# Performance work log

Hardware: AMD Instinct MI355X
Metric: run time of the kernel (lower is better)

Reference implementation:

```python
import jax, jax.numpy as jnp
from jax import lax
import numpy as np

H = 20  # hidden_size


def _lstm_layer(x, Wih, Whh, bih, bhh):
    # x: [B, T, D_in]; Wih: [4H, D_in]; Whh: [4H, H]
    B = x.shape[0]
    b = bih + bhh  # [4H]

    def step(carry, xt):
        h, c = carry
        gates = xt @ Wih.T + h @ Whh.T + b  # [B, 4H]
        i, f, g, o = jnp.split(gates, 4, axis=-1)  # torch gate order: i,f,g,o
        i = jax.nn.sigmoid(i)
        f = jax.nn.sigmoid(f)
        g = jnp.tanh(g)
        o = jax.nn.sigmoid(o)
        c = f * c + i * g
        h = o * jnp.tanh(c)
        return (h, c), h

    h0 = jnp.zeros((B, H), x.dtype)
    c0 = jnp.zeros((B, H), x.dtype)
    (_, _), hs = lax.scan(step, (h0, c0), jnp.swapaxes(x, 0, 1))  # hs: [T, B, H]
    return jnp.swapaxes(hs, 0, 1)  # [B, T, H]


def setup_inputs() -> dict:
    key = jax.random.key(0)
    ks = jax.random.split(key, 11)
    B, T, D = 4096, 512, 1
    s = 1.0 / np.sqrt(H)  # torch LSTM init scale
    u = lambda k, shp: jax.random.uniform(k, shp, jnp.float32, -s, s)
    return {
        "x": jax.random.normal(ks[0], (B, T, D), jnp.float32),
        "Wih0": u(ks[1], (4 * H, D)),
        "Whh0": u(ks[2], (4 * H, H)),
        "bih0": u(ks[3], (4 * H,)),
        "bhh0": u(ks[4], (4 * H,)),
        "Wih1": u(ks[5], (4 * H, H)),
        "Whh1": u(ks[6], (4 * H, H)),
        "bih1": u(ks[7], (4 * H,)),
        "bhh1": u(ks[8], (4 * H,)),
        "fcW": u(ks[9], (1, H)),
        "fcb": u(ks[10], (1,)),
    }


def reference(x, Wih0, Whh0, bih0, bhh0, Wih1, Whh1, bih1, bhh1, fcW, fcb):
    h1 = _lstm_layer(x, Wih0, Whh0, bih0, bhh0)   # [B, T, H]
    h2 = _lstm_layer(h1, Wih1, Whh1, bih1, bhh1)  # [B, T, H]
    # self.drop is defined but never applied in the original forward
    return h2[:, -1, :] @ fcW.T + fcb  # [B, 1]
```

## Files before the change

kernel.cpp:

```cpp
#include <hip/hip_runtime.h>
#include <hip/hip_bf16.h>


namespace {
constexpr int H_  = 20;
constexpr int T_  = 512;
constexpr int B_  = 4096;
constexpr int GPB = 3;

__device__ __forceinline__ float sigm(float v) {
    return 1.0f / (1.0f + __expf(-v));
}
__device__ __forceinline__ float tanh_fast(float v) {
    return 1.0f - 2.0f / (1.0f + __expf(2.0f * v));
}
}

__global__ __launch_bounds__(256, 3) void lstm2_fc_kernel(
    const float* __restrict__ x,
    const float* __restrict__ Wih0, const float* __restrict__ Whh0,
    const float* __restrict__ bih0, const float* __restrict__ bhh0,
    const float* __restrict__ Wih1, const float* __restrict__ Whh1,
    const float* __restrict__ bih1, const float* __restrict__ bhh1,
    const float* __restrict__ fcW,  const float* __restrict__ fcb,
    float* __restrict__ out)
{
    const int tid  = threadIdx.x;
    const int w_s  = __builtin_amdgcn_readfirstlane(tid >> 6);
    const int lane = tid & 63;
    const int g    = lane / H_;
    const int j    = lane - g * H_;
    const int b    = blockIdx.x * GPB + g;
    const bool st  = (g < GPB) && (b < B_);
    const int  gx  = (g < GPB) ? g : (GPB - 1);

    __shared__ float xs[GPB][T_ + 1];
    __shared__ float act0[4][64];
    __shared__ float act1[4][64];
    __shared__ __align__(16) float h0s[4][4][24];
    __shared__ __align__(16) float h1s[4][4][24];

    {
        const int base_b = blockIdx.x * GPB;
        for (int idx = tid; idx < GPB * T_; idx += 256) {
            const int gg  = idx >> 9;
            const int tt  = idx & (T_ - 1);
            int row = base_b + gg; if (row >= B_) row = B_ - 1;
            xs[gg][tt] = x[(size_t)row * T_ + tt];
        }
    }

    const int r = w_s * H_ + j;
    float w0x   = Wih0[r];
    float bias0 = bih0[r] + bhh0[r];
    float bias1 = bih1[r] + bhh1[r];
    float w0h[H_], w1i[H_], w1h[H_];
    #pragma unroll
    for (int k = 0; k < H_; ++k) {
        w0h[k] = Whh0[r * H_ + k];
        w1i[k] = Wih1[r * H_ + k];
        w1h[k] = Whh1[r * H_ + k];
    }
    asm volatile("" : "+v"(w0x), "+v"(bias0), "+v"(bias1));
    #pragma unroll
    for (int k = 0; k < H_; ++k) {
        asm volatile("" : "+v"(w0h[k]), "+v"(w1i[k]), "+v"(w1h[k]));
    }

    float h0r[H_], h1r[H_];
    #pragma unroll
    for (int k = 0; k < H_; ++k) { h0r[k] = 0.0f; h1r[k] = 0.0f; }
    float c0 = 0.0f, c1 = 0.0f;

    float* myAct0 = &act0[w_s][lane];
    float* myAct1 = &act1[w_s][lane];
    const float4* h0row = reinterpret_cast<const float4*>(&h0s[w_s][g][0]);
    const float4* h1row = reinterpret_cast<const float4*>(&h1s[w_s][g][0]);
    const float*  xrow  = &xs[gx][0];

    __syncthreads();
    float xv = xrow[0];

    #pragma unroll 1
    for (int t = 0; t < T_; ++t) {
        float s0 = fmaf(w0x, xv, bias0);
        float s1 = 0.0f, s2 = 0.0f, s3 = 0.0f;
        #pragma unroll
        for (int k = 0; k < H_; k += 4) {
            s0 = fmaf(w0h[k + 0], h0r[k + 0], s0);
            s1 = fmaf(w0h[k + 1], h0r[k + 1], s1);
            s2 = fmaf(w0h[k + 2], h0r[k + 2], s2);
            s3 = fmaf(w0h[k + 3], h0r[k + 3], s3);
        }
        const float gate0 = (s0 + s1) + (s2 + s3);
        float a0;
        if (w_s == 2) a0 = tanh_fast(gate0); else a0 = sigm(gate0);
        *myAct0 = a0;
        const float xnext = xrow[t + 1];
        __syncthreads();
        const float i0 = act0[0][lane];
        const float f0 = act0[1][lane];
        const float z0 = act0[2][lane];
        const float o0 = act0[3][lane];
        c0 = fmaf(f0, c0, i0 * z0);
        const float h0n = o0 * tanh_fast(c0);
        h0s[w_s][g][j] = h0n;

        #pragma unroll
        for (int c4 = 0; c4 < 5; ++c4) {
            const float4 v = h0row[c4];
            h0r[c4 * 4 + 0] = v.x; h0r[c4 * 4 + 1] = v.y;
            h0r[c4 * 4 + 2] = v.z; h0r[c4 * 4 + 3] = v.w;
        }

        float u0 = bias1, u1 = 0.0f, u2 = 0.0f, u3 = 0.0f;
        #pragma unroll
        for (int k = 0; k < H_; k += 2) {
            u0 = fmaf(w1i[k + 0], h0r[k + 0], u0);
            u1 = fmaf(w1i[k + 1], h0r[k + 1], u1);
            u2 = fmaf(w1h[k + 0], h1r[k + 0], u2);
            u3 = fmaf(w1h[k + 1], h1r[k + 1], u3);
        }
        const float gate1 = (u0 + u1) + (u2 + u3);
        float a1;
        if (w_s == 2) a1 = tanh_fast(gate1); else a1 = sigm(gate1);
        *myAct1 = a1;
        __syncthreads();
        const float i1 = act1[0][lane];
        const float f1 = act1[1][lane];
        const float z1 = act1[2][lane];
        const float o1 = act1[3][lane];
        c1 = fmaf(f1, c1, i1 * z1);
        const float h1n = o1 * tanh_fast(c1);
        h1s[w_s][g][j] = h1n;

        #pragma unroll
        for (int c4 = 0; c4 < 5; ++c4) {
            const float4 v = h1row[c4];
            h1r[c4 * 4 + 0] = v.x; h1r[c4 * 4 + 1] = v.y;
            h1r[c4 * 4 + 2] = v.z; h1r[c4 * 4 + 3] = v.w;
        }

        xv = xnext;
    }

    if (w_s == 0 && st && j == 0) {
        float acc = fcb[0];
        #pragma unroll
        for (int k = 0; k < H_; ++k) acc = fmaf(fcW[k], h1r[k], acc);
        out[b] = acc;
    }
}

extern "C" void kernel_launch(void* const* d_in, const int* in_sizes, int n_in,
                              void* d_out, int out_size, void* d_ws, size_t ws_size,
                              hipStream_t stream) {
    const float* x    = (const float*)d_in[0];
    const float* Wih0 = (const float*)d_in[1];
    const float* Whh0 = (const float*)d_in[2];
    const float* bih0 = (const float*)d_in[3];
    const float* bhh0 = (const float*)d_in[4];
    const float* Wih1 = (const float*)d_in[5];
    const float* Whh1 = (const float*)d_in[6];
    const float* bih1 = (const float*)d_in[7];
    const float* bhh1 = (const float*)d_in[8];
    const float* fcW  = (const float*)d_in[9];
    const float* fcb  = (const float*)d_in[10];
    float* out = (float*)d_out;

    const int grid = (B_ + GPB - 1) / GPB;
    lstm2_fc_kernel<<<dim3(grid), dim3(256), 0, stream>>>(
        x, Wih0, Whh0, bih0, bhh0, Wih1, Whh1, bih1, bhh1, fcW, fcb, out);
}
```

Before: 819.8 us.

## Interleave two sequence groups per lane to double ILP and halve grid

Each block now carries six batch rows instead of three. Every lane advances two independent recurrences in lockstep, sharing its register-resident weights across both. The serial per-step chain of FMAs, activations and barriers is amortised over twice the work, and the grid shrinks so all blocks fit in a single resident wave. In exchange the hidden-state registers double, which under the existing launch bounds risks spilling or lower occupancy.

```diff
diff --git a/kernel.cpp b/kernel.cpp
--- a/kernel.cpp
+++ b/kernel.cpp
@@ -6,7 +6,9 @@
 constexpr int H_  = 20;
 constexpr int T_  = 512;
 constexpr int B_  = 4096;
-constexpr int GPB = 3;
+constexpr int PL  = 2;
+constexpr int GRP = 3;
+constexpr int GPB = PL * GRP;
 
 __device__ __forceinline__ float sigm(float v) {
     return 1.0f / (1.0f + __expf(-v));
@@ -30,23 +32,21 @@
     const int lane = tid & 63;
     const int g    = lane / H_;
     const int j    = lane - g * H_;
-    const int b    = blockIdx.x * GPB + g;
-    const bool st  = (g < GPB) && (b < B_);
-    const int  gx  = (g < GPB) ? g : (GPB - 1);
+    const int gx   = (g < GRP) ? g : (GRP - 1);
 
     __shared__ float xs[GPB][T_ + 1];
-    __shared__ float act0[4][64];
-    __shared__ float act1[4][64];
-    __shared__ __align__(16) float h0s[4][4][24];
-    __shared__ __align__(16) float h1s[4][4][24];
+    __shared__ float act0[PL][4][64];
+    __shared__ float act1[PL][4][64];
+    __shared__ __align__(16) float h0s[4][PL][4][28];
+    __shared__ __align__(16) float h1s[4][PL][4][28];
 
     {
         const int base_b = blockIdx.x * GPB;
         for (int idx = tid; idx < GPB * T_; idx += 256) {
-            const int gg  = idx >> 9;
-            const int tt  = idx & (T_ - 1);
-            int row = base_b + gg; if (row >= B_) row = B_ - 1;
-            xs[gg][tt] = x[(size_t)row * T_ + tt];
+            const int ss = idx >> 9;
+            const int tt = idx & (T_ - 1);
+            int row = base_b + ss; if (row >= B_) row = B_ - 1;
+            xs[ss][tt] = x[(size_t)row * T_ + tt];
         }
     }
 
@@ -67,88 +67,123 @@
         asm volatile("" : "+v"(w0h[k]), "+v"(w1i[k]), "+v"(w1h[k]));
     }
 
-    float h0r[H_], h1r[H_];
+    float h0r[PL][H_], h1r[PL][H_];
+    float c0[PL], c1[PL];
     #pragma unroll
-    for (int k = 0; k < H_; ++k) { h0r[k] = 0.0f; h1r[k] = 0.0f; }
-    float c0 = 0.0f, c1 = 0.0f;
-
-    float* myAct0 = &act0[w_s][lane];
-    float* myAct1 = &act1[w_s][lane];
-    const float4* h0row = reinterpret_cast<const float4*>(&h0s[w_s][g][0]);
-    const float4* h1row = reinterpret_cast<const float4*>(&h1s[w_s][g][0]);
-    const float*  xrow  = &xs[gx][0];
+    for (int p = 0; p < PL; ++p) {
+        c0[p] = 0.0f; c1[p] = 0.0f;
+        #pragma unroll
+        for (int k = 0; k < H_; ++k) { h0r[p][k] = 0.0f; h1r[p][k] = 0.0f; }
+    }
+
+    const float* xrow0 = &xs[0 * GRP + gx][0];
+    const float* xrow1 = &xs[1 * GRP + gx][0];
 
     __syncthreads();
-    float xv = xrow[0];
+    float xv[PL] = { xrow0[0], xrow1[0] };
 
     #pragma unroll 1
     for (int t = 0; t < T_; ++t) {
-        float s0 = fmaf(w0x, xv, bias0);
-        float s1 = 0.0f, s2 = 0.0f, s3 = 0.0f;
+        float s[PL][4];
+        #pragma unroll
+        for (int p = 0; p < PL; ++p) {
+            s[p][0] = fmaf(w0x, xv[p], bias0);
+            s[p][1] = 0.0f; s[p][2] = 0.0f; s[p][3] = 0.0f;
+        }
         #pragma unroll
         for (int k = 0; k < H_; k += 4) {
-            s0 = fmaf(w0h[k + 0], h0r[k + 0], s0);
-            s1 = fmaf(w0h[k + 1], h0r[k + 1], s1);
-            s2 = fmaf(w0h[k + 2], h0r[k + 2], s2);
-            s3 = fmaf(w0h[k + 3], h0r[k + 3], s3);
-        }
-        const float gate0 = (s0 + s1) + (s2 + s3);
-        float a0;
-        if (w_s == 2) a0 = tanh_fast(gate0); else a0 = sigm(gate0);
-        *myAct0 = a0;
-        const float xnext = xrow[t + 1];
+            #pragma unroll
+            for (int q = 0; q < 4; ++q) {
+                const float wk = w0h[k + q];
+                s[0][q] = fmaf(wk, h0r[0][k + q], s[0][q]);
+                s[1][q] = fmaf(wk, h0r[1][k + q], s[1][q]);
+            }
+        }
+        #pragma unroll
+        for (int p = 0; p < PL; ++p) {
+            const float gate = (s[p][0] + s[p][1]) + (s[p][2] + s[p][3]);
+            const float a = (w_s == 2) ? tanh_fast(gate) : sigm(gate);
+            act0[p][w_s][lane] = a;
+        }
+        const float xn0 = xrow0[t + 1];
+        const float xn1 = xrow1[t + 1];
         __syncthreads();
-        const float i0 = act0[0][lane];
-        const float f0 = act0[1][lane];
-        const float z0 = act0[2][lane];
-        const float o0 = act0[3][lane];
-        c0 = fmaf(f0, c0, i0 * z0);
-        const float h0n = o0 * tanh_fast(c0);
-        h0s[w_s][g][j] = h0n;
-
-        #pragma unroll
-        for (int c4 = 0; c4 < 5; ++c4) {
-            const float4 v = h0row[c4];
-            h0r[c4 * 4 + 0] = v.x; h0r[c4 * 4 + 1] = v.y;
-            h0r[c4 * 4 + 2] = v.z; h0r[c4 * 4 + 3] = v.w;
-        }
-
-        float u0 = bias1, u1 = 0.0f, u2 = 0.0f, u3 = 0.0f;
+
+        #pragma unroll
+        for (int p = 0; p < PL; ++p) {
+            const float i0 = act0[p][0][lane];
+            const float f0 = act0[p][1][lane];
+            const float z0 = act0[p][2][lane];
+            const float o0 = act0[p][3][lane];
+            c0[p] = fmaf(f0, c0[p], i0 * z0);
+            const float hn = o0 * tanh_fast(c0[p]);
+            h0s[w_s][p][g][j] = hn;
+            const float4* rp = reinterpret_cast<const float4*>(&h0s[w_s][p][gx][0]);
+            #pragma unroll
+            for (int c4 = 0; c4 < 5; ++c4) {
+                const float4 v = rp[c4];
+                h0r[p][c4*4+0] = v.x; h0r[p][c4*4+1] = v.y;
+                h0r[p][c4*4+2] = v.z; h0r[p][c4*4+3] = v.w;
+            }
+        }
+
+        float u[PL][4];
+        #pragma unroll
+        for (int p = 0; p < PL; ++p) {
+            u[p][0] = bias1; u[p][1] = 0.0f; u[p][2] = 0.0f; u[p][3] = 0.0f;
+        }
         #pragma unroll
         for (int k = 0; k < H_; k += 2) {
-            u0 = fmaf(w1i[k + 0], h0r[k + 0], u0);
-            u1 = fmaf(w1i[k + 1], h0r[k + 1], u1);
-            u2 = fmaf(w1h[k + 0], h1r[k + 0], u2);
-            u3 = fmaf(w1h[k + 1], h1r[k + 1], u3);
-        }
-        const float gate1 = (u0 + u1) + (u2 + u3);
-        float a1;
-        if (w_s == 2) a1 = tanh_fast(gate1); else a1 = sigm(gate1);
-        *myAct1 = a1;
+            const float wa0 = w1i[k + 0], wa1 = w1i[k + 1];
+            const float wb0 = w1h[k + 0], wb1 = w1h[k + 1];
+            #pragma unroll
+            for (int p = 0; p < PL; ++p) {
+                u[p][0] = fmaf(wa0, h0r[p][k + 0], u[p][0]);
+                u[p][1] = fmaf(wa1, h0r[p][k + 1], u[p][1]);
+                u[p][2] = fmaf(wb0, h1r[p][k + 0], u[p][2]);
+                u[p][3] = fmaf(wb1, h1r[p][k + 1], u[p][3]);
+            }
+        }
+        #pragma unroll
+        for (int p = 0; p < PL; ++p) {
+            const float gate = (u[p][0] + u[p][1]) + (u[p][2] + u[p][3]);
+            const float a = (w_s == 2) ? tanh_fast(gate) : sigm(gate);
+            act1[p][w_s][lane] = a;
+        }
         __syncthreads();
-        const float i1 = act1[0][lane];
-        const float f1 = act1[1][lane];
-        const float z1 = act1[2][lane];
-        const float o1 = act1[3][lane];
-        c1 = fmaf(f1, c1, i1 * z1);
-        const float h1n = o1 * tanh_fast(c1);
-        h1s[w_s][g][j] = h1n;
-
-        #pragma unroll
-        for (int c4 = 0; c4 < 5; ++c4) {
-            const float4 v = h1row[c4];
-            h1r[c4 * 4 + 0] = v.x; h1r[c4 * 4 + 1] = v.y;
-            h1r[c4 * 4 + 2] = v.z; h1r[c4 * 4 + 3] = v.w;
-        }
-
-        xv = xnext;
-    }
-
-    if (w_s == 0 && st && j == 0) {
-        float acc = fcb[0];
-        #pragma unroll
-        for (int k = 0; k < H_; ++k) acc = fmaf(fcW[k], h1r[k], acc);
-        out[b] = acc;
+
+        #pragma unroll
+        for (int p = 0; p < PL; ++p) {
+            const float i1 = act1[p][0][lane];
+            const float f1 = act1[p][1][lane];
+            const float z1 = act1[p][2][lane];
+            const float o1 = act1[p][3][lane];
+            c1[p] = fmaf(f1, c1[p], i1 * z1);
+            const float hn = o1 * tanh_fast(c1[p]);
+            h1s[w_s][p][g][j] = hn;
+            const float4* rp = reinterpret_cast<const float4*>(&h1s[w_s][p][gx][0]);
+            #pragma unroll
+            for (int c4 = 0; c4 < 5; ++c4) {
+                const float4 v = rp[c4];
+                h1r[p][c4*4+0] = v.x; h1r[p][c4*4+1] = v.y;
+                h1r[p][c4*4+2] = v.z; h1r[p][c4*4+3] = v.w;
+            }
+        }
+
+        xv[0] = xn0; xv[1] = xn1;
+    }
+
+    if (w_s == 0 && g < GRP && j == 0) {
+        #pragma unroll
+        for (int p = 0; p < PL; ++p) {
+            const int b = blockIdx.x * GPB + p * GRP + g;
+            if (b < B_) {
+                float acc = fcb[0];
+                #pragma unroll
+                for (int k = 0; k < H_; ++k) acc = fmaf(fcW[k], h1r[p][k], acc);
+                out[b] = acc;
+            }
+        }
     }
 }
 
```

After: 884.4 us. +7.9%, slower.

## Skew layer-1 by one step to share a single barrier per timestep

Applied to the files above, without the earlier changes.

Layer 1 now runs one timestep behind layer 0, so both layers' gate dot products and activations are computed together and exchanged with one __syncthreads per step instead of two. Activation buffers are double-buffered by step parity, and the loop runs one extra iteration with the first layer-1 cell state masked to zero. Sigmoid and tanh also switch from IEEE division to the hardware reciprocal. The aim is to halve barrier count and add ILP on the serial recurrence, at the cost of an extra iteration and slightly less accurate reciprocal.

```diff
diff --git a/kernel.cpp b/kernel.cpp
--- a/kernel.cpp
+++ b/kernel.cpp
@@ -8,11 +8,14 @@
 constexpr int B_  = 4096;
 constexpr int GPB = 3;
 
+__device__ __forceinline__ float rcp_fast(float v) {
+    return __builtin_amdgcn_rcpf(v);
+}
 __device__ __forceinline__ float sigm(float v) {
-    return 1.0f / (1.0f + __expf(-v));
+    return rcp_fast(1.0f + __expf(-v));
 }
 __device__ __forceinline__ float tanh_fast(float v) {
-    return 1.0f - 2.0f / (1.0f + __expf(2.0f * v));
+    return fmaf(-2.0f, rcp_fast(1.0f + __expf(2.0f * v)), 1.0f);
 }
 }
 
@@ -34,20 +37,21 @@
     const bool st  = (g < GPB) && (b < B_);
     const int  gx  = (g < GPB) ? g : (GPB - 1);
 
-    __shared__ float xs[GPB][T_ + 1];
-    __shared__ float act0[4][64];
-    __shared__ float act1[4][64];
-    __shared__ __align__(16) float h0s[4][4][24];
-    __shared__ __align__(16) float h1s[4][4][24];
+    __shared__ float xs[GPB][T_ + 2];
+    __shared__ float act0[2][4][64];
+    __shared__ float act1[2][4][64];
+    __shared__ __align__(16) float h0s[4][4][28];
+    __shared__ __align__(16) float h1s[4][4][28];
 
     {
         const int base_b = blockIdx.x * GPB;
         for (int idx = tid; idx < GPB * T_; idx += 256) {
-            const int gg  = idx >> 9;
-            const int tt  = idx & (T_ - 1);
+            const int gg = idx >> 9;
+            const int tt = idx & (T_ - 1);
             int row = base_b + gg; if (row >= B_) row = B_ - 1;
             xs[gg][tt] = x[(size_t)row * T_ + tt];
         }
+        if (tid < GPB * 2) xs[tid >> 1][T_ + (tid & 1)] = 0.0f;
     }
 
     const int r = w_s * H_ + j;
@@ -72,73 +76,69 @@
     for (int k = 0; k < H_; ++k) { h0r[k] = 0.0f; h1r[k] = 0.0f; }
     float c0 = 0.0f, c1 = 0.0f;
 
-    float* myAct0 = &act0[w_s][lane];
-    float* myAct1 = &act1[w_s][lane];
-    const float4* h0row = reinterpret_cast<const float4*>(&h0s[w_s][g][0]);
-    const float4* h1row = reinterpret_cast<const float4*>(&h1s[w_s][g][0]);
+    const float4* h0row = reinterpret_cast<const float4*>(&h0s[w_s][gx][0]);
+    const float4* h1row = reinterpret_cast<const float4*>(&h1s[w_s][gx][0]);
     const float*  xrow  = &xs[gx][0];
 
     __syncthreads();
     float xv = xrow[0];
 
     #pragma unroll 1
-    for (int t = 0; t < T_; ++t) {
+    for (int t = 0; t <= T_; ++t) {
+        const int par = t & 1;
         float s0 = fmaf(w0x, xv, bias0);
         float s1 = 0.0f, s2 = 0.0f, s3 = 0.0f;
+        float u0 = bias1, u1 = 0.0f, u2 = 0.0f, u3 = 0.0f;
         #pragma unroll
         for (int k = 0; k < H_; k += 4) {
             s0 = fmaf(w0h[k + 0], h0r[k + 0], s0);
             s1 = fmaf(w0h[k + 1], h0r[k + 1], s1);
             s2 = fmaf(w0h[k + 2], h0r[k + 2], s2);
             s3 = fmaf(w0h[k + 3], h0r[k + 3], s3);
-        }
-        const float gate0 = (s0 + s1) + (s2 + s3);
-        float a0;
-        if (w_s == 2) a0 = tanh_fast(gate0); else a0 = sigm(gate0);
-        *myAct0 = a0;
-        const float xnext = xrow[t + 1];
-        __syncthreads();
-        const float i0 = act0[0][lane];
-        const float f0 = act0[1][lane];
-        const float z0 = act0[2][lane];
-        const float o0 = act0[3][lane];
-        c0 = fmaf(f0, c0, i0 * z0);
-        const float h0n = o0 * tanh_fast(c0);
-        h0s[w_s][g][j] = h0n;
-
-        #pragma unroll
-        for (int c4 = 0; c4 < 5; ++c4) {
-            const float4 v = h0row[c4];
-            h0r[c4 * 4 + 0] = v.x; h0r[c4 * 4 + 1] = v.y;
-            h0r[c4 * 4 + 2] = v.z; h0r[c4 * 4 + 3] = v.w;
-        }
-
-        float u0 = bias1, u1 = 0.0f, u2 = 0.0f, u3 = 0.0f;
-        #pragma unroll
-        for (int k = 0; k < H_; k += 2) {
             u0 = fmaf(w1i[k + 0], h0r[k + 0], u0);
             u1 = fmaf(w1i[k + 1], h0r[k + 1], u1);
             u2 = fmaf(w1h[k + 0], h1r[k + 0], u2);
             u3 = fmaf(w1h[k + 1], h1r[k + 1], u3);
+            u0 = fmaf(w1i[k + 2], h0r[k + 2], u0);
+            u1 = fmaf(w1i[k + 3], h0r[k + 3], u1);
+            u2 = fmaf(w1h[k + 2], h1r[k + 2], u2);
+            u3 = fmaf(w1h[k + 3], h1r[k + 3], u3);
         }
+        const float gate0 = (s0 + s1) + (s2 + s3);
         const float gate1 = (u0 + u1) + (u2 + u3);
-        float a1;
-        if (w_s == 2) a1 = tanh_fast(gate1); else a1 = sigm(gate1);
-        *myAct1 = a1;
+        float a0, a1;
+        if (w_s == 2) { a0 = tanh_fast(gate0); a1 = tanh_fast(gate1); }
+        else          { a0 = sigm(gate0);      a1 = sigm(gate1); }
+        act0[par][w_s][lane] = a0;
+        act1[par][w_s][lane] = a1;
+        const float xnext = xrow[t + 1];
         __syncthreads();
-        const float i1 = act1[0][lane];
-        const float f1 = act1[1][lane];
-        const float z1 = act1[2][lane];
-        const float o1 = act1[3][lane];
-        c1 = fmaf(f1, c1, i1 * z1);
+
+        const float i0 = act0[par][0][lane];
+        const float f0 = act0[par][1][lane];
+        const float z0 = act0[par][2][lane];
+        const float o0 = act0[par][3][lane];
+        const float i1 = act1[par][0][lane];
+        const float f1 = act1[par][1][lane];
+        const float z1 = act1[par][2][lane];
+        const float o1 = act1[par][3][lane];
+
+        c0 = fmaf(f0, c0, i0 * z0);
+        const float h0n = o0 * tanh_fast(c0);
+        const float keep = (t == 0) ? 0.0f : 1.0f;
+        c1 = fmaf(f1, c1, i1 * z1) * keep;
         const float h1n = o1 * tanh_fast(c1);
+
+        h0s[w_s][g][j] = h0n;
         h1s[w_s][g][j] = h1n;
-
         #pragma unroll
         for (int c4 = 0; c4 < 5; ++c4) {
-            const float4 v = h1row[c4];
-            h1r[c4 * 4 + 0] = v.x; h1r[c4 * 4 + 1] = v.y;
-            h1r[c4 * 4 + 2] = v.z; h1r[c4 * 4 + 3] = v.w;
+            const float4 v0 = h0row[c4];
+            h0r[c4*4+0] = v0.x; h0r[c4*4+1] = v0.y;
+            h0r[c4*4+2] = v0.z; h0r[c4*4+3] = v0.w;
+            const float4 v1 = h1row[c4];
+            h1r[c4*4+0] = v1.x; h1r[c4*4+1] = v1.y;
+            h1r[c4*4+2] = v1.z; h1r[c4*4+3] = v1.w;
         }
 
         xv = xnext;
```

New measurement: 718.3 us. 1.14x faster.
